# Optimization experiments

Measured on AMD Instinct MI355X. Metric: run time of the kernel, lower is better.

Reference implementation:

```python
import jax, jax.numpy as jnp
import numpy as np

S, B, H = 2048, 32, 1024

def setup_inputs() -> dict:
    key = jax.random.key(0)
    ks = jax.random.split(key, 5)
    hidden = jax.random.normal(ks[0], (B, H), dtype=jnp.float32)
    encoder_outputs = jax.random.normal(ks[1], (S, B, H), dtype=jnp.float32)
    source_lengths = jax.random.randint(ks[2], (B,), 1, S + 1, dtype=jnp.int32)
    attn_w = jax.random.normal(ks[3], (H, 2 * H), dtype=jnp.float32) / np.sqrt(2 * H)
    attn_b = jnp.zeros((H,), dtype=jnp.float32)
    v = jax.random.uniform(ks[4], (H,), dtype=jnp.float32)
    return {"hidden": hidden, "encoder_outputs": encoder_outputs,
            "source_lengths": source_lengths, "attn_w": attn_w,
            "attn_b": attn_b, "v": v}

def reference(hidden, encoder_outputs, source_lengths, attn_w, attn_b, v):
    s, b, h = encoder_outputs.shape
    # Broadcast decoder hidden over source positions: (S,B,H)
    hid = jnp.broadcast_to(hidden[None, :, :], (s, b, h))
    cat = jnp.concatenate([hid, encoder_outputs], axis=2)          # (S,B,2H)
    energy = jnp.tanh(jnp.einsum('sbk,hk->sbh', cat, attn_w) + attn_b)  # (S,B,H)
    scores = jnp.einsum('sbh,h->bs', energy, v)                     # (B,S)
    mask = jnp.arange(s)[None, :] < source_lengths[:, None]         # (B,S)
    scores = jnp.where(mask, scores, jnp.float32(-1e10))
    attention_weights = jax.nn.softmax(scores, axis=1)              # (B,S)
    context = jnp.einsum('bs,sbh->bh', attention_weights, encoder_outputs)
    return context, attention_weights
```

## Files before the change

### kernel.cpp

```cpp
#include <hip/hip_runtime.h>

#define S_DIM 2048
#define B_DIM 32
#define H_DIM 1024
#define ROWS  (S_DIM * B_DIM)

typedef __attribute__((ext_vector_type(8))) short s16x8;
typedef __attribute__((ext_vector_type(4))) float f32x4;


__device__ __forceinline__ unsigned pack2_bf16(float a, float b) {
  unsigned ua = __float_as_uint(a) + 0x8000u;
  unsigned ub = __float_as_uint(b) + 0x8000u;
  return __builtin_amdgcn_perm(ub, ua, 0x07060302u);
}

__device__ __forceinline__ unsigned short bf16_rne(float f) {
  unsigned u = __float_as_uint(f);
  return (unsigned short)((u + 0x7FFFu + ((u >> 16) & 1u)) >> 16);
}

__device__ __forceinline__ float fast_tanh(float x) {
  x = fminf(15.0f, fmaxf(-15.0f, x));
  float z = __expf(-2.0f * x);
  return (1.0f - z) * __builtin_amdgcn_rcpf(1.0f + z);
}

__device__ __forceinline__ void load_lds16(const void* g, void* l) {
  __builtin_amdgcn_global_load_lds(
      (const __attribute__((address_space(1))) unsigned int*)g,
      (__attribute__((address_space(3))) unsigned int*)l, 16, 0, 0);
}

__global__ void hidproj_kernel(const float* __restrict__ hidden,
                               const float* __restrict__ attn_w,
                               const float* __restrict__ attn_b,
                               float* __restrict__ hp) {
  int b  = blockIdx.y;
  int hl = threadIdx.x & 63;
  int h  = blockIdx.x * 64 + hl;
  int kp = threadIdx.x >> 6;
  const f32x4* wrow = (const f32x4*)(attn_w + (size_t)h * (2 * H_DIM)) + kp * 64;
  const f32x4* xrow = (const f32x4*)(hidden + (size_t)b * H_DIM) + kp * 64;
  float s = 0.f;
#pragma unroll 8
  for (int k = 0; k < 64; ++k) {
    f32x4 w = wrow[k], x = xrow[k];
    s = fmaf(w.x, x.x, s); s = fmaf(w.y, x.y, s);
    s = fmaf(w.z, x.z, s); s = fmaf(w.w, x.w, s);
  }
  __shared__ float red[4][64];
  red[kp][hl] = s;
  __syncthreads();
  if (kp == 0) {
    float t = red[0][hl] + red[1][hl] + red[2][hl] + red[3][hl] + attn_b[h];
    hp[(size_t)b * H_DIM + h] = t;
  }
}

__global__ void packW2_kernel(const float* __restrict__ attn_w,
                              unsigned short* __restrict__ Bp) {
  int idx = blockIdx.x * 256 + threadIdx.x;
  int h  = idx >> 8;
  int kc = idx & 255;
  f32x4 w = *(const f32x4*)(attn_w + (size_t)h * (2 * H_DIM) + H_DIM + kc * 4);
  ushort4 o;
  o.x = bf16_rne(w.x); o.y = bf16_rne(w.y); o.z = bf16_rne(w.z); o.w = bf16_rne(w.w);
  *(ushort4*)(Bp + (size_t)h * H_DIM + kc * 4) = o;
}

__global__ __launch_bounds__(256, 2)
void gemm_scores_kernel(const float* __restrict__ enc,
                        const unsigned short* __restrict__ Bp,
                        const float* __restrict__ hp,
                        const float* __restrict__ v,
                        float* __restrict__ scores) {
  __shared__ __align__(16) float As[8][128][4];
  __shared__ __align__(16) unsigned short Bs[256][32];
  const int tid  = threadIdx.x;
  const int lane = tid & 63;
  const int wid  = tid >> 6;
  const int wm   = wid >> 1;
  const int wn   = wid & 1;
  const int m16  = lane & 15;
  const int quad = lane >> 4;
  const int row0 = blockIdx.y * 128;
  const int n0   = blockIdx.x * 256;

  f32x4 acc[4][8];
#pragma unroll
  for (int i = 0; i < 4; ++i)
#pragma unroll
    for (int j = 0; j < 8; ++j) acc[i][j] = (f32x4){0.f, 0.f, 0.f, 0.f};

  for (int k0 = 0; k0 < H_DIM; k0 += 32) {
#pragma unroll
    for (int c = 0; c < 4; ++c) {
      int q  = c * 256 + tid;
      int r  = q & 127;
      int kc = q >> 7;
      load_lds16(enc + (size_t)(row0 + r) * H_DIM + k0 + kc * 4, &As[kc][r][0]);
      int n  = q >> 2;
      int kb = q & 3;
      load_lds16(Bp + (size_t)(n0 + n) * H_DIM + k0 + kb * 8, &Bs[n][kb * 8]);
    }
    __syncthreads();

    s16x8 af[4], bf[8];
#pragma unroll
    for (int mf = 0; mf < 4; ++mf) {
      int r = wm * 64 + mf * 16 + m16;
      f32x4 a0 = *(const f32x4*)&As[quad * 2][r][0];
      f32x4 a1 = *(const f32x4*)&As[quad * 2 + 1][r][0];
      union { s16x8 v8; unsigned u[4]; } pk;
      pk.u[0] = pack2_bf16(a0.x, a0.y);
      pk.u[1] = pack2_bf16(a0.z, a0.w);
      pk.u[2] = pack2_bf16(a1.x, a1.y);
      pk.u[3] = pack2_bf16(a1.z, a1.w);
      af[mf] = pk.v8;
    }
#pragma unroll
    for (int nf = 0; nf < 8; ++nf) {
      int n = wn * 128 + nf * 16 + m16;
      bf[nf] = *(const s16x8*)&Bs[n][quad * 8];
    }
#pragma unroll
    for (int mf = 0; mf < 4; ++mf)
#pragma unroll
      for (int nf = 0; nf < 8; ++nf)
        acc[mf][nf] = __builtin_amdgcn_mfma_f32_16x16x32_bf16(
            af[mf], bf[nf], acc[mf][nf], 0, 0, 0);
    __syncthreads();
  }

#pragma unroll
  for (int mf = 0; mf < 4; ++mf) {
#pragma unroll
    for (int reg = 0; reg < 4; ++reg) {
      int rl    = wm * 64 + mf * 16 + quad * 4 + reg;
      int row_g = row0 + rl;
      int b     = row_g & 31;
      int s     = row_g >> 5;
      float psum = 0.f;
#pragma unroll
      for (int nf = 0; nf < 8; ++nf) {
        int col = n0 + wn * 128 + nf * 16 + m16;
        float e = acc[mf][nf][reg] + hp[b * H_DIM + col];
        e = fast_tanh(e);
        psum = fmaf(e, v[col], psum);
      }
      psum += __shfl_xor(psum, 1);
      psum += __shfl_xor(psum, 2);
      psum += __shfl_xor(psum, 4);
      psum += __shfl_xor(psum, 8);
      if (m16 == 0) atomicAdd(&scores[b * S_DIM + s], psum);
    }
  }
}

__global__ void softmax_kernel(const float* __restrict__ scores,
                               const int* __restrict__ lens,
                               float* __restrict__ wout) {
  int b = blockIdx.x, tid = threadIdx.x;
  int len = lens[b];
  float vals[8];
  float m = -3.0e38f;
#pragma unroll
  for (int i = 0; i < 8; ++i) {
    int s = i * 256 + tid;
    float x = scores[b * S_DIM + s];
    vals[i] = (s < len) ? x : -3.0e38f;
    m = fmaxf(m, vals[i]);
  }
#pragma unroll
  for (int off = 32; off > 0; off >>= 1) m = fmaxf(m, __shfl_xor(m, off));
  __shared__ float redm[4], reds[4];
  int wid = tid >> 6, lane = tid & 63;
  if (lane == 0) redm[wid] = m;
  __syncthreads();
  m = fmaxf(fmaxf(redm[0], redm[1]), fmaxf(redm[2], redm[3]));

  float e[8];
  float sum = 0.f;
#pragma unroll
  for (int i = 0; i < 8; ++i) {
    int s = i * 256 + tid;
    e[i] = (s < len) ? __expf(vals[i] - m) : 0.f;
    sum += e[i];
  }
#pragma unroll
  for (int off = 32; off > 0; off >>= 1) sum += __shfl_xor(sum, off);
  if (lane == 0) reds[wid] = sum;
  __syncthreads();
  sum = reds[0] + reds[1] + reds[2] + reds[3];
  float inv = 1.0f / sum;
#pragma unroll
  for (int i = 0; i < 8; ++i)
    wout[b * S_DIM + i * 256 + tid] = e[i] * inv;
}

__global__ void context_kernel(const float* __restrict__ enc,
                               const float* __restrict__ wts,
                               float* __restrict__ ctx) {
  int sc = blockIdx.x;
  int b  = blockIdx.y;
  int tid = threadIdx.x;
  f32x4 acc = (f32x4){0.f, 0.f, 0.f, 0.f};
  const float* wrow = wts + (size_t)b * S_DIM + sc * 64;
  for (int i = 0; i < 64; ++i) {
    float w = wrow[i];
    if (w != 0.0f) {
      f32x4 ev = *(const f32x4*)(enc + ((size_t)(sc * 64 + i) * B_DIM + b) * H_DIM + tid * 4);
      acc.x = fmaf(w, ev.x, acc.x);
      acc.y = fmaf(w, ev.y, acc.y);
      acc.z = fmaf(w, ev.z, acc.z);
      acc.w = fmaf(w, ev.w, acc.w);
    }
  }
  float* dst = ctx + (size_t)b * H_DIM + tid * 4;
  atomicAdd(dst + 0, acc.x);
  atomicAdd(dst + 1, acc.y);
  atomicAdd(dst + 2, acc.z);
  atomicAdd(dst + 3, acc.w);
}

extern "C" void kernel_launch(void* const* d_in, const int* in_sizes, int n_in,
                              void* d_out, int out_size, void* d_ws, size_t ws_size,
                              hipStream_t stream) {
  const float* hidden = (const float*)d_in[0];
  const float* enc    = (const float*)d_in[1];
  const int*   lens   = (const int*)d_in[2];
  const float* attn_w = (const float*)d_in[3];
  const float* attn_b = (const float*)d_in[4];
  const float* v      = (const float*)d_in[5];

  float* out_ctx = (float*)d_out;
  float* out_w   = (float*)d_out + B_DIM * H_DIM;

  float* scores = (float*)d_ws;
  float* hp     = scores + B_DIM * S_DIM;
  unsigned short* Bp = (unsigned short*)(hp + B_DIM * H_DIM);

  hipMemsetAsync(scores, 0, (size_t)B_DIM * S_DIM * sizeof(float), stream);
  hipMemsetAsync(out_ctx, 0, (size_t)B_DIM * H_DIM * sizeof(float), stream);

  hipLaunchKernelGGL(hidproj_kernel, dim3(H_DIM / 64, B_DIM), dim3(256), 0, stream,
                     hidden, attn_w, attn_b, hp);
  hipLaunchKernelGGL(packW2_kernel, dim3((H_DIM * H_DIM / 4) / 256), dim3(256), 0, stream,
                     attn_w, Bp);
  hipLaunchKernelGGL(gemm_scores_kernel, dim3(H_DIM / 256, ROWS / 128), dim3(256), 0, stream,
                     enc, Bp, hp, v, scores);
  hipLaunchKernelGGL(softmax_kernel, dim3(B_DIM), dim3(256), 0, stream,
                     scores, lens, out_w);
  hipLaunchKernelGGL(context_kernel, dim3(S_DIM / 64, B_DIM), dim3(256), 0, stream,
                     enc, out_w, out_ctx);
}
```

Before: 714.8 us.

## Pre-convert encoder outputs to bf16 and reshape GEMM to 512-thread blocks

Measured after the change: 854.2 us. 19.5% more time.

```diff
diff --git a/kernel.cpp b/kernel.cpp
--- a/kernel.cpp
+++ b/kernel.cpp
@@ -20,6 +20,10 @@
   return (unsigned short)((u + 0x7FFFu + ((u >> 16) & 1u)) >> 16);
 }
 
+__device__ __forceinline__ float bf16_to_f32(unsigned short s) {
+  return __uint_as_float((unsigned)s << 16);
+}
+
 __device__ __forceinline__ float fast_tanh(float x) {
   x = fminf(15.0f, fmaxf(-15.0f, x));
   float z = __expf(-2.0f * x);
@@ -32,29 +36,45 @@
       (__attribute__((address_space(3))) unsigned int*)l, 16, 0, 0);
 }
 
+__global__ void conv_bf16_kernel(const float* __restrict__ enc,
+                                 unsigned short* __restrict__ Ep) {
+  size_t idx = (size_t)blockIdx.x * 256 + threadIdx.x;
+  size_t base = idx * 8;
+  f32x4 a0 = *(const f32x4*)(enc + base);
+  f32x4 a1 = *(const f32x4*)(enc + base + 4);
+  union { s16x8 v; unsigned short u[8]; } o;
+  o.u[0] = bf16_rne(a0.x); o.u[1] = bf16_rne(a0.y);
+  o.u[2] = bf16_rne(a0.z); o.u[3] = bf16_rne(a0.w);
+  o.u[4] = bf16_rne(a1.x); o.u[5] = bf16_rne(a1.y);
+  o.u[6] = bf16_rne(a1.z); o.u[7] = bf16_rne(a1.w);
+  *(s16x8*)(Ep + base) = o.v;
+}
+
 __global__ void hidproj_kernel(const float* __restrict__ hidden,
                                const float* __restrict__ attn_w,
                                const float* __restrict__ attn_b,
                                float* __restrict__ hp) {
-  int b  = blockIdx.y;
-  int hl = threadIdx.x & 63;
-  int h  = blockIdx.x * 64 + hl;
-  int kp = threadIdx.x >> 6;
-  const f32x4* wrow = (const f32x4*)(attn_w + (size_t)h * (2 * H_DIM)) + kp * 64;
-  const f32x4* xrow = (const f32x4*)(hidden + (size_t)b * H_DIM) + kp * 64;
-  float s = 0.f;
-#pragma unroll 8
-  for (int k = 0; k < 64; ++k) {
-    f32x4 w = wrow[k], x = xrow[k];
-    s = fmaf(w.x, x.x, s); s = fmaf(w.y, x.y, s);
-    s = fmaf(w.z, x.z, s); s = fmaf(w.w, x.w, s);
-  }
-  __shared__ float red[4][64];
-  red[kp][hl] = s;
-  __syncthreads();
-  if (kp == 0) {
-    float t = red[0][hl] + red[1][hl] + red[2][hl] + red[3][hl] + attn_b[h];
-    hp[(size_t)b * H_DIM + h] = t;
+  int tid = threadIdx.x;
+  int hl  = tid >> 4;
+  int kp  = tid & 15;
+  int h   = blockIdx.x * 16 + hl;
+  const f32x4* wrow = (const f32x4*)(attn_w + (size_t)h * (2 * H_DIM)) + kp * 16;
+  f32x4 w[16];
+#pragma unroll
+  for (int j = 0; j < 16; ++j) w[j] = wrow[j];
+  float bias = attn_b[h];
+  for (int b = 0; b < B_DIM; ++b) {
+    const f32x4* xrow = (const f32x4*)(hidden + (size_t)b * H_DIM) + kp * 16;
+    float s = 0.f;
+#pragma unroll
+    for (int j = 0; j < 16; ++j) {
+      f32x4 x = xrow[j];
+      s = fmaf(w[j].x, x.x, s); s = fmaf(w[j].y, x.y, s);
+      s = fmaf(w[j].z, x.z, s); s = fmaf(w[j].w, x.w, s);
+    }
+    s += __shfl_xor(s, 1); s += __shfl_xor(s, 2);
+    s += __shfl_xor(s, 4); s += __shfl_xor(s, 8);
+    if (kp == 0) hp[(size_t)b * H_DIM + h] = s + bias;
   }
 }
 
@@ -69,65 +89,79 @@
   *(ushort4*)(Bp + (size_t)h * H_DIM + kc * 4) = o;
 }
 
-__global__ __launch_bounds__(256, 2)
-void gemm_scores_kernel(const float* __restrict__ enc,
+template <bool ABF16>
+__global__ __launch_bounds__(512, 4)
+void gemm_scores_kernel(const float* __restrict__ encf,
+                        const unsigned short* __restrict__ encb,
                         const unsigned short* __restrict__ Bp,
                         const float* __restrict__ hp,
                         const float* __restrict__ v,
                         float* __restrict__ scores) {
-  __shared__ __align__(16) float As[8][128][4];
-  __shared__ __align__(16) unsigned short Bs[256][32];
+  __shared__ __align__(16) unsigned short Bs[4][256][8];
+  __shared__ __align__(16) char AsRaw[ABF16 ? 8192 : 16384];
+  auto* As16 = (unsigned short(*)[128][8])AsRaw;
+  auto* As32 = (float(*)[128][4])AsRaw;
+
   const int tid  = threadIdx.x;
   const int lane = tid & 63;
   const int wid  = tid >> 6;
-  const int wm   = wid >> 1;
-  const int wn   = wid & 1;
+  const int wm   = wid >> 2;
+  const int wn   = wid & 3;
   const int m16  = lane & 15;
   const int quad = lane >> 4;
   const int row0 = blockIdx.y * 128;
   const int n0   = blockIdx.x * 256;
 
-  f32x4 acc[4][8];
+  f32x4 acc[4][4];
 #pragma unroll
   for (int i = 0; i < 4; ++i)
 #pragma unroll
-    for (int j = 0; j < 8; ++j) acc[i][j] = (f32x4){0.f, 0.f, 0.f, 0.f};
+    for (int j = 0; j < 4; ++j) acc[i][j] = (f32x4){0.f, 0.f, 0.f, 0.f};
 
   for (int k0 = 0; k0 < H_DIM; k0 += 32) {
-#pragma unroll
-    for (int c = 0; c < 4; ++c) {
-      int q  = c * 256 + tid;
-      int r  = q & 127;
-      int kc = q >> 7;
-      load_lds16(enc + (size_t)(row0 + r) * H_DIM + k0 + kc * 4, &As[kc][r][0]);
-      int n  = q >> 2;
-      int kb = q & 3;
-      load_lds16(Bp + (size_t)(n0 + n) * H_DIM + k0 + kb * 8, &Bs[n][kb * 8]);
+    if constexpr (ABF16) {
+      int r = tid & 127, kc = tid >> 7;
+      load_lds16(encb + (size_t)(row0 + r) * H_DIM + k0 + kc * 8, &As16[kc][r][0]);
+    } else {
+#pragma unroll
+      for (int c = 0; c < 2; ++c) {
+        int q = c * 512 + tid, r = q & 127, kc = q >> 7;
+        load_lds16(encf + (size_t)(row0 + r) * H_DIM + k0 + kc * 4, &As32[kc][r][0]);
+      }
+    }
+#pragma unroll
+    for (int c = 0; c < 2; ++c) {
+      int q = c * 512 + tid, n = q & 255, kb = q >> 8;
+      load_lds16(Bp + (size_t)(n0 + n) * H_DIM + k0 + kb * 8, &Bs[kb][n][0]);
     }
     __syncthreads();
 
-    s16x8 af[4], bf[8];
+    s16x8 af[4], bf[4];
 #pragma unroll
     for (int mf = 0; mf < 4; ++mf) {
       int r = wm * 64 + mf * 16 + m16;
-      f32x4 a0 = *(const f32x4*)&As[quad * 2][r][0];
-      f32x4 a1 = *(const f32x4*)&As[quad * 2 + 1][r][0];
-      union { s16x8 v8; unsigned u[4]; } pk;
-      pk.u[0] = pack2_bf16(a0.x, a0.y);
-      pk.u[1] = pack2_bf16(a0.z, a0.w);
-      pk.u[2] = pack2_bf16(a1.x, a1.y);
-      pk.u[3] = pack2_bf16(a1.z, a1.w);
-      af[mf] = pk.v8;
-    }
-#pragma unroll
-    for (int nf = 0; nf < 8; ++nf) {
-      int n = wn * 128 + nf * 16 + m16;
-      bf[nf] = *(const s16x8*)&Bs[n][quad * 8];
+      if constexpr (ABF16) {
+        af[mf] = *(const s16x8*)&As16[quad][r][0];
+      } else {
+        f32x4 a0 = *(const f32x4*)&As32[quad * 2][r][0];
+        f32x4 a1 = *(const f32x4*)&As32[quad * 2 + 1][r][0];
+        union { s16x8 v8; unsigned u[4]; } pk;
+        pk.u[0] = pack2_bf16(a0.x, a0.y);
+        pk.u[1] = pack2_bf16(a0.z, a0.w);
+        pk.u[2] = pack2_bf16(a1.x, a1.y);
+        pk.u[3] = pack2_bf16(a1.z, a1.w);
+        af[mf] = pk.v8;
+      }
+    }
+#pragma unroll
+    for (int nf = 0; nf < 4; ++nf) {
+      int n = wn * 64 + nf * 16 + m16;
+      bf[nf] = *(const s16x8*)&Bs[quad][n][0];
     }
 #pragma unroll
     for (int mf = 0; mf < 4; ++mf)
 #pragma unroll
-      for (int nf = 0; nf < 8; ++nf)
+      for (int nf = 0; nf < 4; ++nf)
         acc[mf][nf] = __builtin_amdgcn_mfma_f32_16x16x32_bf16(
             af[mf], bf[nf], acc[mf][nf], 0, 0, 0);
     __syncthreads();
@@ -137,14 +171,13 @@
   for (int mf = 0; mf < 4; ++mf) {
 #pragma unroll
     for (int reg = 0; reg < 4; ++reg) {
-      int rl    = wm * 64 + mf * 16 + quad * 4 + reg;
-      int row_g = row0 + rl;
+      int row_g = row0 + wm * 64 + mf * 16 + quad * 4 + reg;
       int b     = row_g & 31;
       int s     = row_g >> 5;
       float psum = 0.f;
 #pragma unroll
-      for (int nf = 0; nf < 8; ++nf) {
-        int col = n0 + wn * 128 + nf * 16 + m16;
+      for (int nf = 0; nf < 4; ++nf) {
+        int col = n0 + wn * 64 + nf * 16 + m16;
         float e = acc[mf][nf][reg] + hp[b * H_DIM + col];
         e = fast_tanh(e);
         psum = fmaf(e, v[col], psum);
@@ -199,22 +232,37 @@
     wout[b * S_DIM + i * 256 + tid] = e[i] * inv;
 }
 
-__global__ void context_kernel(const float* __restrict__ enc,
+template <bool BF16>
+__global__ void context_kernel(const float* __restrict__ encf,
+                               const unsigned short* __restrict__ encb,
                                const float* __restrict__ wts,
+                               const int* __restrict__ lens,
                                float* __restrict__ ctx) {
   int sc = blockIdx.x;
   int b  = blockIdx.y;
+  int len = lens[b];
+  int s0 = sc * 64;
+  if (s0 >= len) return;
+  int cnt = min(64, len - s0);
   int tid = threadIdx.x;
   f32x4 acc = (f32x4){0.f, 0.f, 0.f, 0.f};
-  const float* wrow = wts + (size_t)b * S_DIM + sc * 64;
-  for (int i = 0; i < 64; ++i) {
+  const float* wrow = wts + (size_t)b * S_DIM + s0;
+#pragma unroll 4
+  for (int i = 0; i < cnt; ++i) {
     float w = wrow[i];
-    if (w != 0.0f) {
-      f32x4 ev = *(const f32x4*)(enc + ((size_t)(sc * 64 + i) * B_DIM + b) * H_DIM + tid * 4);
-      acc.x = fmaf(w, ev.x, acc.x);
-      acc.y = fmaf(w, ev.y, acc.y);
-      acc.z = fmaf(w, ev.z, acc.z);
-      acc.w = fmaf(w, ev.w, acc.w);
+    size_t base = ((size_t)(s0 + i) * B_DIM + b) * H_DIM + tid * 4;
+    if constexpr (BF16) {
+      ushort4 e = *(const ushort4*)(encb + base);
+      acc.x = fmaf(w, bf16_to_f32(e.x), acc.x);
+      acc.y = fmaf(w, bf16_to_f32(e.y), acc.y);
+      acc.z = fmaf(w, bf16_to_f32(e.z), acc.z);
+      acc.w = fmaf(w, bf16_to_f32(e.w), acc.w);
+    } else {
+      f32x4 e = *(const f32x4*)(encf + base);
+      acc.x = fmaf(w, e.x, acc.x);
+      acc.y = fmaf(w, e.y, acc.y);
+      acc.z = fmaf(w, e.z, acc.z);
+      acc.w = fmaf(w, e.w, acc.w);
     }
   }
   float* dst = ctx + (size_t)b * H_DIM + tid * 4;
@@ -237,21 +285,41 @@
   float* out_ctx = (float*)d_out;
   float* out_w   = (float*)d_out + B_DIM * H_DIM;
 
-  float* scores = (float*)d_ws;
-  float* hp     = scores + B_DIM * S_DIM;
-  unsigned short* Bp = (unsigned short*)(hp + B_DIM * H_DIM);
-
-  hipMemsetAsync(scores, 0, (size_t)B_DIM * S_DIM * sizeof(float), stream);
+  const size_t epBytes = (size_t)ROWS * H_DIM * 2;
+  const size_t scBytes = (size_t)B_DIM * S_DIM * 4;
+  const size_t hpBytes = (size_t)B_DIM * H_DIM * 4;
+  const size_t bpBytes = (size_t)H_DIM * H_DIM * 2;
+  bool bf16path = ws_size >= epBytes + scBytes + hpBytes + bpBytes + 256;
+
+  char* p = (char*)d_ws;
+  unsigned short* Ep = nullptr;
+  if (bf16path) { Ep = (unsigned short*)p; p += epBytes; }
+  float* scores = (float*)p; p += scBytes;
+  float* hp     = (float*)p; p += hpBytes;
+  unsigned short* Bp = (unsigned short*)p;
+
+  hipMemsetAsync(scores, 0, scBytes, stream);
   hipMemsetAsync(out_ctx, 0, (size_t)B_DIM * H_DIM * sizeof(float), stream);
 
-  hipLaunchKernelGGL(hidproj_kernel, dim3(H_DIM / 64, B_DIM), dim3(256), 0, stream,
+  if (bf16path)
+    hipLaunchKernelGGL(conv_bf16_kernel, dim3(ROWS * H_DIM / 8 / 256), dim3(256),
+                       0, stream, enc, Ep);
+  hipLaunchKernelGGL(hidproj_kernel, dim3(H_DIM / 16), dim3(256), 0, stream,
                      hidden, attn_w, attn_b, hp);
-  hipLaunchKernelGGL(packW2_kernel, dim3((H_DIM * H_DIM / 4) / 256), dim3(256), 0, stream,
-                     attn_w, Bp);
-  hipLaunchKernelGGL(gemm_scores_kernel, dim3(H_DIM / 256, ROWS / 128), dim3(256), 0, stream,
-                     enc, Bp, hp, v, scores);
+  hipLaunchKernelGGL(packW2_kernel, dim3((H_DIM * H_DIM / 4) / 256), dim3(256),
+                     0, stream, attn_w, Bp);
+  if (bf16path)
+    hipLaunchKernelGGL((gemm_scores_kernel<true>), dim3(H_DIM / 256, ROWS / 128),
+                       dim3(512), 0, stream, enc, Ep, Bp, hp, v, scores);
+  else
+    hipLaunchKernelGGL((gemm_scores_kernel<false>), dim3(H_DIM / 256, ROWS / 128),
+                       dim3(512), 0, stream, enc, Ep, Bp, hp, v, scores);
   hipLaunchKernelGGL(softmax_kernel, dim3(B_DIM), dim3(256), 0, stream,
                      scores, lens, out_w);
-  hipLaunchKernelGGL(context_kernel, dim3(S_DIM / 64, B_DIM), dim3(256), 0, stream,
-                     enc, out_w, out_ctx);
-}
+  if (bf16path)
+    hipLaunchKernelGGL((context_kernel<true>), dim3(S_DIM / 64, B_DIM), dim3(256),
+                       0, stream, enc, Ep, out_w, lens, out_ctx);
+  else
+    hipLaunchKernelGGL((context_kernel<false>), dim3(S_DIM / 64, B_DIM), dim3(256),
+                       0, stream, enc, Ep, out_w, lens, out_ctx);
+}
```
